# Performance work log

Hardware: AMD Instinct MI355X
Metric: run time of the kernel (lower is better)

Reference implementation:

```python
import jax, jax.numpy as jnp
import numpy as np

T = 64      # sequence_length / rolling_size
B = 256     # batch
XD = 128    # x_dim
HD = 1024   # h_dim
SKIP = 5    # frozen skip_size (torch code draws random.randint(1,10) at init)


def _make_masks(rs, n):
    # Mirrors: W1=randint(0,1); W2=1 if W1==0 else randint(0,1)
    masks = []
    for _ in range(n):
        w1 = int(rs.randint(0, 2))
        w2 = 1 if w1 == 0 else int(rs.randint(0, 2))
        masks.append((float(w1), float(w2)))
    return masks

_RS = np.random.RandomState(0)
ENC_MASKS = _make_masks(_RS, T)  # encoder constructed first in RAE.__init__
DEC_MASKS = _make_masks(_RS, T)


def _gru_cell(x, h, W_ih, W_hh, b_ih, b_hh):
    # torch.nn.GRUCell semantics
    gi = x @ W_ih.T + b_ih            # [B, 3H]
    gh = h @ W_hh.T + b_hh            # [B, 3H]
    i_r, i_z, i_n = jnp.split(gi, 3, axis=1)
    h_r, h_z, h_n = jnp.split(gh, 3, axis=1)
    r = jax.nn.sigmoid(i_r + h_r)
    z = jax.nn.sigmoid(i_z + h_z)
    n = jnp.tanh(i_n + r * h_n)
    return (1.0 - z) * n + z * h


def setup_inputs() -> dict:
    key = jax.random.key(0)
    ks = jax.random.split(key, 12)
    s = 0.05
    return {
        "input": jax.random.normal(ks[0], (B, T, XD), jnp.float32),
        "enc_W_ih": jax.random.normal(ks[1], (3 * HD, XD), jnp.float32) * s,
        "enc_W_hh": jax.random.normal(ks[2], (3 * HD, HD), jnp.float32) * s,
        "enc_b_ih": jax.random.normal(ks[3], (3 * HD,), jnp.float32) * s,
        "enc_b_hh": jax.random.normal(ks[4], (3 * HD,), jnp.float32) * s,
        "dec_W_ih": jax.random.normal(ks[5], (3 * HD, XD), jnp.float32) * s,
        "dec_W_hh": jax.random.normal(ks[6], (3 * HD, HD), jnp.float32) * s,
        "dec_b_ih": jax.random.normal(ks[7], (3 * HD,), jnp.float32) * s,
        "dec_b_hh": jax.random.normal(ks[8], (3 * HD,), jnp.float32) * s,
        "lin_W": jax.random.normal(ks[9], (XD, HD), jnp.float32) * s,
        "lin_b": jax.random.normal(ks[10], (XD,), jnp.float32) * s,
    }


def reference(input, enc_W_ih, enc_W_hh, enc_b_ih, enc_b_hh,
              dec_W_ih, dec_W_hh, dec_b_ih, dec_b_hh, lin_W, lin_b):
    Bn = input.shape[0]
    zeros_h = jnp.zeros((Bn, HD), input.dtype)

    # ---- Encoder: masked-skip GRU recurrence (list semantics match torch) ----
    h_origs = [zeros_h]
    h_skips = [zeros_h] * SKIP
    for i in range(T):
        h_prev = h_origs[i] * ENC_MASKS[i][0] + h_skips[i - SKIP] * ENC_MASKS[i][1]
        h_new = _gru_cell(input[:, i], h_prev, enc_W_ih, enc_W_hh, enc_b_ih, enc_b_hh)
        h_origs.append(h_new)
        h_skips.append(h_new)  # chunk(repeat(1,2)) gives two identical copies
    h_enc = h_origs[-1] + h_skips[-1]

    # ---- Decoder: feeds back its own projected output ----
    GO = jnp.zeros((Bn, XD), input.dtype)
    h_origs = [h_enc]
    h_skips = [zeros_h] * SKIP
    outputs = []
    for i in range(T):
        x_in = GO if i == 0 else outputs[i - 1]
        h_prev = h_origs[i] * DEC_MASKS[i][0] + h_skips[i - SKIP] * DEC_MASKS[i][1]
        h_new = _gru_cell(x_in, h_prev, dec_W_ih, dec_W_hh, dec_b_ih, dec_b_hh)
        h_origs.append(h_new)
        h_skips.append(h_new)
        # torch projects AFTER the appends, using h_origs[i] (pre-update state)
        proj = (h_origs[i] + h_skips[i - SKIP]) @ lin_W.T + lin_b
        outputs.append(proj)

    return jnp.stack(outputs, axis=1)  # [B, T, XD], matches permute(1,0,2)
```

## Files before the change

kernel.cpp:

```cpp
#include <hip/hip_runtime.h>
#include <cstdint>
#include <cstddef>

#define XDIM 128
#define HDIM 1024
#define ORS 8192
#define NPH 129

typedef __attribute__((ext_vector_type(8))) short short8;
typedef __attribute__((ext_vector_type(4))) float f32x4;

static const size_t GSTRIDE = (size_t)36 * 64 * 64 * 8;
static const size_t EPACK   = 4 * GSTRIDE;

struct Phase {
  float spA, spB, nsA, nsB, qsA, qsB, q2sA, q2sB;
  int ebase, xe, xd, afrag;
  int hpA, hpB, nskip, qskip, q2skip;
  int anext, pnext, p2next, hout;
  int pfrag, pouti, pxout;
};
static_assert(sizeof(Phase) == 96, "phase size");

__device__ __forceinline__ unsigned short f2bf(float f) {
  union { float f; unsigned u; } c; c.f = f;
  unsigned u = c.u + (0x7fffu + ((c.u >> 16) & 1u));
  return (unsigned short)(u >> 16);
}
__device__ __forceinline__ float sigm_(float x) { return 1.f / (1.f + __expf(-x)); }
__device__ __forceinline__ float tanh_(float x) { return 2.f / (1.f + __expf(-2.f * x)) - 1.f; }

__device__ __forceinline__ short8 cvt8(float4 a, float4 b) {
  short8 o;
  o[0] = (short)f2bf(a.x); o[1] = (short)f2bf(a.y); o[2] = (short)f2bf(a.z); o[3] = (short)f2bf(a.w);
  o[4] = (short)f2bf(b.x); o[5] = (short)f2bf(b.y); o[6] = (short)f2bf(b.z); o[7] = (short)f2bf(b.w);
  return o;
}

__device__ __forceinline__ unsigned long long ld64_sys(const unsigned short* p) {
  return __hip_atomic_load((const unsigned long long*)p, __ATOMIC_RELAXED,
                           __HIP_MEMORY_SCOPE_SYSTEM);
}
__device__ __forceinline__ unsigned ld32_sys(const unsigned* p) {
  return __hip_atomic_load(p, __ATOMIC_RELAXED, __HIP_MEMORY_SCOPE_SYSTEM);
}
__device__ __forceinline__ void st32_sys(unsigned* p, unsigned v) {
  __hip_atomic_store(p, v, __ATOMIC_RELAXED, __HIP_MEMORY_SCOPE_SYSTEM);
}
union U128 { unsigned long long u[2]; short8 v; };
__device__ __forceinline__ short8 mk8(unsigned long long a, unsigned long long b) {
  U128 u; u.u[0] = a; u.u[1] = b; return u.v;
}
__device__ __forceinline__ void st_pair_bf(unsigned short* addr, int lane, unsigned short v) {
  unsigned other = (unsigned)__shfl_xor((int)(unsigned)v, 1);
  if ((lane & 1) == 0)
    st32_sys((unsigned*)addr, ((unsigned)v & 0xffffu) | (other << 16));
}

#define MFMA(a,b,c) __builtin_amdgcn_mfma_f32_16x16x32_bf16((a),(b),(c),0,0,0)

__global__ __launch_bounds__(256) void pack_gates(
    const float* __restrict__ eWih, const float* __restrict__ eWhh,
    const float* __restrict__ dWih, const float* __restrict__ dWhh,
    short* __restrict__ Bg)
{
  unsigned t = blockIdx.x * 256u + threadIdx.x;
  unsigned l  = t & 63u; t >>= 6;
  unsigned nf = t & 63u; t >>= 6;
  unsigned ks = t % 36u; t /= 36u;
  unsigned g  = t & 3u;  t >>= 2;
  if (t >= 2u) return;
  if ((g == 2u && ks >= 4u) || (g == 3u && ks < 4u)) return;
  const float* Wih = t ? dWih : eWih;
  const float* Whh = t ? dWhh : eWhh;
  int k = (int)(ks * 32u + (l >> 4) * 8u);
  int n = (int)(nf * 16u + (l & 15u));
  const float* src;
  if (g == 3u)      src = Whh + (size_t)(2048 + n) * HDIM + (k - XDIM);
  else if (g == 2u) src = Wih + (size_t)(2048 + n) * XDIM + k;
  else if (ks < 4u) src = Wih + (size_t)(g * HDIM + n) * XDIM + k;
  else              src = Whh + (size_t)(g * HDIM + n) * HDIM + (k - XDIM);
  float4 a = *(const float4*)src;
  float4 b = *(const float4*)(src + 4);
  size_t off = ((((size_t)t * 4u + g) * 36u + ks) * 64u + nf) * 64u + l;
  *(short8*)(Bg + off * 8u) = cvt8(a, b);
}

__global__ __launch_bounds__(256) void pack_lin(const float* __restrict__ linW,
                                                short* __restrict__ Bl)
{
  unsigned t = blockIdx.x * 256u + threadIdx.x;
  unsigned l  = t & 63u; t >>= 6;
  unsigned nf = t & 7u;  t >>= 3;
  unsigned ks = t;
  if (ks >= 32u) return;
  int k = (int)(ks * 32u + (l >> 4) * 8u);
  int n = (int)(nf * 16u + (l & 15u));
  const float* src = linW + (size_t)n * HDIM + k;
  float4 a = *(const float4*)src;
  float4 b = *(const float4*)(src + 4);
  *(short8*)(Bl + (((size_t)ks * 8u + nf) * 64u + l) * 8u) = cvt8(a, b);
}

__global__ __launch_bounds__(256) void pack_bias(
    const float* __restrict__ eIh, const float* __restrict__ eHh,
    const float* __restrict__ dIh, const float* __restrict__ dHh,
    float* __restrict__ bias)
{
  unsigned t = blockIdx.x * 256u + threadIdx.x;
  if (t >= 8192u) return;
  unsigned n = t & 1023u, g = (t >> 10) & 3u, e = t >> 12;
  const float* bih = e ? dIh : eIh;
  const float* bhh = e ? dHh : eHh;
  float v;
  if (g == 0u)      v = bih[n] + bhh[n];
  else if (g == 1u) v = bih[HDIM + n] + bhh[HDIM + n];
  else if (g == 2u) v = bih[2 * HDIM + n];
  else              v = bhh[2 * HDIM + n];
  bias[t] = v;
}

__global__ __launch_bounds__(256) void pack_x(const float* __restrict__ in,
                                              unsigned short* __restrict__ Xe)
{
  unsigned t = blockIdx.x * 256u + threadIdx.x;
  unsigned row = t & 255u; t >>= 8;
  unsigned lq  = t & 3u;   t >>= 2;
  unsigned ks  = t & 3u;   t >>= 2;
  unsigned i   = t;
  if (i >= 64u) return;
  const float* src = in + (size_t)row * ORS + i * 128u + ks * 32u + lq * 8u;
  float4 a = *(const float4*)src;
  float4 b = *(const float4*)(src + 4);
  *(short8*)(Xe + ((((size_t)i * 4u + ks) * 4u + lq) * 256u + row) * 8u) = cvt8(a, b);
}

__device__ __forceinline__ int mkslot(int s) { return s % 12; }

__device__ void blank_phase(Phase& ph) {
  ph.spA = ph.spB = ph.nsA = ph.nsB = ph.qsA = ph.qsB = ph.q2sA = ph.q2sB = 0.f;
  ph.ebase = 0; ph.xe = -1; ph.xd = -1; ph.afrag = -1;
  ph.hpA = ph.hpB = ph.nskip = ph.qskip = ph.q2skip = 0;
  ph.anext = ph.pnext = ph.p2next = -1; ph.hout = -1;
  ph.pfrag = -1; ph.pouti = -1; ph.pxout = -1;
}

__global__ void setup_phases(Phase* __restrict__ phs, unsigned* __restrict__ arr) {
  const int t = threadIdx.x;
  for (int k = t; k < 1024; k += 64) arr[k] = 0u;
  if (t != 0) return;

  unsigned mt[624];
  mt[0] = 0u;
  for (int i = 1; i < 624; ++i)
    mt[i] = 1812433253u * (mt[i - 1] ^ (mt[i - 1] >> 30)) + (unsigned)i;
  for (int i = 0; i < 624; ++i) {
    unsigned y = (mt[i] & 0x80000000u) | (mt[(i + 1) % 624] & 0x7fffffffu);
    unsigned v = mt[(i + 397) % 624] ^ (y >> 1);
    mt[i] = (y & 1u) ? (v ^ 0x9908b0dfu) : v;
  }
  int mti = 0;
  float ew[64][2], dw[64][2];
  for (int e = 0; e < 2; ++e) {
    for (int i = 0; i < 64; ++i) {
      unsigned y = mt[mti++];
      y ^= y >> 11; y ^= (y << 7) & 0x9d2c5680u; y ^= (y << 15) & 0xefc60000u; y ^= y >> 18;
      int w1 = (int)(y & 1u);
      int w2 = 1;
      if (w1 != 0) {
        unsigned z = mt[mti++];
        z ^= z >> 11; z ^= (z << 7) & 0x9d2c5680u; z ^= (z << 15) & 0xefc60000u; z ^= z >> 18;
        w2 = (int)(z & 1u);
      }
      if (e == 0) { ew[i][0] = (float)w1; ew[i][1] = (float)w2; }
      else        { dw[i][0] = (float)w1; dw[i][1] = (float)w2; }
    }
  }

  bool anull = true;
  for (int i = 0; i < 64; ++i) {
    Phase ph; blank_phase(ph);
    ph.ebase = 0; ph.xe = i;
    ph.hout = mkslot(i);
    if (i >= 1 && !anull) ph.afrag = i & 3;
    ph.hpA = mkslot(i >= 1 ? i - 1 : 0);
    ph.spA = i ? ew[i][0] : 0.f;
    if (i == 3)       { ph.hpB = mkslot(1);      ph.spB = ew[i][1]; }
    else if (i == 4)  { ph.hpB = mkslot(3);      ph.spB = ew[i][1]; }
    else if (i >= 10) { ph.hpB = mkslot(i - 10); ph.spB = ew[i][1]; }
    if (i < 63) {
      int n = i + 1;
      ph.anext = n & 3;
      if (n == 4) ph.nsA = ew[4][0] + ew[4][1];
      else {
        ph.nsA = ew[n][0];
        if (n == 3)       { ph.nsB = ew[3][1]; ph.nskip = mkslot(1); }
        else if (n >= 10) { ph.nsB = ew[n][1]; ph.nskip = mkslot(n - 10); }
      }
    } else {
      ph.anext = 0; ph.nsA = 2.f * dw[0][0];
      ph.pnext = 0; ph.qsA = 2.f;
    }
    if (ph.anext >= 0) {
      anull = (ph.nsA == 0.f && ph.nsB == 0.f);
      if (anull) ph.anext = -1;
    }
    phs[i] = ph;
  }
  for (int i = 0; i < 64; ++i) {
    int p = 64 + i + (i >= 5 ? 1 : 0);
    int s = 64 + i;
    Phase ph; blank_phase(ph);
    ph.ebase = 1;
    ph.xd = i ? (i - 1) & 3 : -1;
    ph.hout = mkslot(s);
    if (!anull) ph.afrag = i & 3;
    ph.hpA = mkslot(i ? s - 1 : 63);
    ph.spA = i ? dw[i][0] : 2.f * dw[0][0];
    if (i == 3)       { ph.hpB = mkslot(64 + 1);  ph.spB = dw[i][1]; }
    else if (i == 4)  { ph.hpB = mkslot(64 + 3);  ph.spB = dw[i][1]; }
    else if (i >= 10) { ph.hpB = mkslot(s - 10);  ph.spB = dw[i][1]; }
    if (i < 63) {
      int n = i + 1;
      ph.anext = n & 3;
      if (n == 4) ph.nsA = dw[4][0] + dw[4][1];
      else {
        ph.nsA = dw[n][0];
        if (n == 3)       { ph.nsB = dw[3][1]; ph.nskip = mkslot(64 + 1); }
        else if (n >= 10) { ph.nsB = dw[n][1]; ph.nskip = mkslot(64 + n - 10); }
      }
    }
    if (i == 2)      { ph.pnext = 3; ph.qsA = 2.f; }
    else if (i == 3) {  }
    else if (i == 4) { ph.pnext = 1; ph.qsA = 1.f;
                       ph.p2next = 0; ph.q2sA = 1.f; ph.q2sB = 1.f;
                       ph.q2skip = mkslot(64 + 3); }
    else if (i < 63) {
      int n = i + 1;
      ph.pnext = n & 3; ph.qsA = 1.f;
      if (n == 2)       { ph.qsB = 1.f; ph.qskip = mkslot(64 + 0); }
      else if (n >= 10) { ph.qsB = 1.f; ph.qskip = mkslot(64 + n - 10); }
    }
    if (ph.anext >= 0) {
      bool z = (ph.nsA == 0.f && ph.nsB == 0.f);
      if (z) ph.anext = -1;
      anull = z;
    }
    if (i != 4) { ph.pfrag = i & 3; ph.pouti = i; ph.pxout = i & 3; }
    phs[p] = ph;
    if (i == 4) {
      Phase pp; blank_phase(pp);
      pp.ebase = 1;
      pp.pfrag = 0; pp.pouti = 4; pp.pxout = 0;
      phs[69] = pp;
    }
  }
}

__global__ __launch_bounds__(512, 2) void rae_persist(
    const Phase* __restrict__ phs,
    const unsigned short* __restrict__ Xe,
    const unsigned short* __restrict__ BgE,
    const unsigned short* __restrict__ BgD,
    const unsigned short* __restrict__ Blin,
    const float* __restrict__ bias,
    const float* __restrict__ linb,
    float* __restrict__ hring,
    unsigned short* __restrict__ AnB,
    unsigned short* __restrict__ PnB,
    unsigned short* __restrict__ XdB,
    float* __restrict__ out,
    unsigned* __restrict__ arr)
{
  const int tid = threadIdx.x;
  const int lane = tid & 63;
  const int wave = tid >> 6;
  const int l15 = lane & 15, lq = lane >> 4;
  const int bid = blockIdx.x;
  const int mt = bid >> 5, ns = bid & 31;
  const int nf0 = ns * 2;
  const int R0 = mt * 32;
  const int hu0 = (wave < 4) ? wave + 8 : wave;

  __shared__ f32x4 red[8][2][6][64];
  __shared__ f32x4 red2[4][2][2][64];
  __shared__ f32x4 red3[8][2][64];
  __shared__ Phase lph[NPH];

  for (int idx = tid; idx < NPH * (int)(sizeof(Phase) / 4); idx += 512)
    ((int*)lph)[idx] = ((const int*)phs)[idx];
  __syncthreads();

#pragma unroll 1
  for (int p = 0; p < NPH; ++p) {
    const Phase& ph = lph[p];
    const bool cell = (ph.hout >= 0);
    const bool proj = (ph.pfrag >= 0) && (ns < 8);
    const unsigned short* Bg = ph.ebase ? BgD : BgE;
    const float* bias4 = bias + (ph.ebase ? 4096 : 0);

    const f32x4 zero = {0.f, 0.f, 0.f, 0.f};
    f32x4 acc[2][6];
    f32x4 g2a[2][2];
#pragma unroll
    for (int rf = 0; rf < 2; ++rf) {
#pragma unroll
      for (int s = 0; s < 6; ++s) acc[rf][s] = zero;
      g2a[rf][0] = zero; g2a[rf][1] = zero;
    }

    auto do_x = [&](const unsigned short* xf, bool sys) {
      const unsigned short* bb = Bg + ((size_t)(wave * 64 + nf0) * 64 + lane) * 8;
      short8 b00 = *(const short8*)(bb);
      short8 b01 = *(const short8*)(bb + 512);
      short8 b10 = *(const short8*)(bb + GSTRIDE);
      short8 b11 = *(const short8*)(bb + GSTRIDE + 512);
      short8 b20 = *(const short8*)(bb + 2 * GSTRIDE);
      short8 b21 = *(const short8*)(bb + 2 * GSTRIDE + 512);
#pragma unroll
      for (int rf = 0; rf < 2; ++rf) {
        const unsigned short* a = xf + (((size_t)(wave * 4 + lq)) * 256 + R0 + rf * 16 + l15) * 8;
        short8 av;
        if (sys) av = mk8(ld64_sys(a), ld64_sys(a + 4));
        else     av = *(const short8*)a;
        acc[rf][0] = MFMA(av, b00, acc[rf][0]);
        acc[rf][1] = MFMA(av, b01, acc[rf][1]);
        acc[rf][2] = MFMA(av, b10, acc[rf][2]);
        acc[rf][3] = MFMA(av, b11, acc[rf][3]);
        g2a[rf][0] = MFMA(av, b20, g2a[rf][0]);
        g2a[rf][1] = MFMA(av, b21, g2a[rf][1]);
      }
    };

    float hpv[4] = {0,0,0,0}, nskv[4] = {0,0,0,0},
          qskv[4] = {0,0,0,0}, q2skv[4] = {0,0,0,0};
    if (cell && wave < 4) {
      const int erf = wave >> 1, enf = wave & 1;
      const int colE = ns * 32 + enf * 16 + l15;
      const float* hpA = hring + (size_t)ph.hpA * 262144u;
      const float* hpB = hring + (size_t)ph.hpB * 262144u;
      const float* nsk = hring + (size_t)ph.nskip * 262144u;
      const float* qsk = hring + (size_t)ph.qskip * 262144u;
      const float* q2k = hring + (size_t)ph.q2skip * 262144u;
#pragma unroll
      for (int q = 0; q < 4; ++q) {
        const size_t o = (size_t)(R0 + erf * 16 + lq * 4 + q) * HDIM + colE;
        float hv = 0.f;
        if (ph.spA != 0.f) hv = ph.spA * hpA[o];
        if (ph.spB != 0.f) hv = fmaf(ph.spB, hpB[o], hv);
        hpv[q] = hv;
        if (ph.anext >= 0 && ph.nsB != 0.f) nskv[q] = nsk[o];
        if (ph.pnext >= 0 && ph.qsB != 0.f) qskv[q] = qsk[o];
        if (ph.p2next >= 0) q2skv[q] = q2k[o];
      }
    }
    if (cell && wave < 4 && ph.xe >= 0)
      do_x(Xe + (size_t)ph.xe * 32768u, false);

    if (p > 0) {
      int guard = 0;
      for (;;) {
        unsigned v = ld32_sys(&arr[(mt << 5) + (lane & 31)]);
        if (__all(v >= (unsigned)p)) break;
        if (++guard > (1 << 22)) break;
      }
    }

    if (cell && wave < 4 && ph.xd >= 0)
      do_x(XdB + (size_t)ph.xd * 32768u, true);

    if (cell && ph.afrag >= 0) {
      const unsigned short* af = AnB + (size_t)ph.afrag * 262144u;
      unsigned long long ha0[4][2], ha1[4][2];
#pragma unroll
      for (int k = 0; k < 4; ++k) {
        const int u = hu0 + 8 * k;
#pragma unroll
        for (int rf = 0; rf < 2; ++rf) {
          const unsigned short* b =
              af + (((size_t)((u - 4) * 4 + lq)) * 256 + R0 + rf * 16 + l15) * 8;
          ha0[k][rf] = ld64_sys(b); ha1[k][rf] = ld64_sys(b + 4);
        }
      }
#pragma unroll
      for (int k = 0; k < 4; ++k) {
        const int u = hu0 + 8 * k;
        const unsigned short* bb = Bg + ((size_t)(u * 64 + nf0) * 64 + lane) * 8;
        short8 b00 = *(const short8*)(bb);
        short8 b01 = *(const short8*)(bb + 512);
        short8 b10 = *(const short8*)(bb + GSTRIDE);
        short8 b11 = *(const short8*)(bb + GSTRIDE + 512);
        short8 b30 = *(const short8*)(bb + 3 * GSTRIDE);
        short8 b31 = *(const short8*)(bb + 3 * GSTRIDE + 512);
#pragma unroll
        for (int rf = 0; rf < 2; ++rf) {
          short8 av = mk8(ha0[k][rf], ha1[k][rf]);
          acc[rf][0] = MFMA(av, b00, acc[rf][0]);
          acc[rf][1] = MFMA(av, b01, acc[rf][1]);
          acc[rf][2] = MFMA(av, b10, acc[rf][2]);
          acc[rf][3] = MFMA(av, b11, acc[rf][3]);
          acc[rf][4] = MFMA(av, b30, acc[rf][4]);
          acc[rf][5] = MFMA(av, b31, acc[rf][5]);
        }
      }
    }

    if (cell) {
#pragma unroll
      for (int rf = 0; rf < 2; ++rf) {
#pragma unroll
        for (int s = 0; s < 6; ++s) red[wave][rf][s][lane] = acc[rf][s];
      }
      if (wave < 4) {
#pragma unroll
        for (int rf = 0; rf < 2; ++rf) {
          red2[wave][rf][0][lane] = g2a[rf][0];
          red2[wave][rf][1][lane] = g2a[rf][1];
        }
      }
    }
    __syncthreads();

    if (cell && wave < 4) {
      const int erf = wave >> 1, enf = wave & 1;
      f32x4 S0 = zero, S1 = zero, S3 = zero, S2 = zero;
#pragma unroll
      for (int w = 0; w < 8; ++w) {
        S0 += red[w][erf][0 + enf][lane];
        S1 += red[w][erf][2 + enf][lane];
        S3 += red[w][erf][4 + enf][lane];
      }
#pragma unroll
      for (int w = 0; w < 4; ++w) S2 += red2[w][erf][enf][lane];
      const int colE = ns * 32 + enf * 16 + l15;
      const float br = bias4[colE],            bz = bias4[HDIM + colE];
      const float bi = bias4[2 * HDIM + colE], bh = bias4[3 * HDIM + colE];
      const int fa = (colE >> 3) * 2048 + (colE & 7);
      float* hout = hring + (size_t)ph.hout * 262144u;
      unsigned short* anx = ph.anext  >= 0 ? AnB + (size_t)ph.anext  * 262144u : nullptr;
      unsigned short* pnx = ph.pnext  >= 0 ? PnB + (size_t)ph.pnext  * 262144u : nullptr;
      unsigned short* p2x = ph.p2next >= 0 ? PnB + (size_t)ph.p2next * 262144u : nullptr;
#pragma unroll
      for (int q = 0; q < 4; ++q) {
        const int row = R0 + erf * 16 + lq * 4 + q;
        const float r  = sigm_(S0[q] + br);
        const float z  = sigm_(S1[q] + bz);
        const float nv = tanh_(S2[q] + bi + r * (S3[q] + bh));
        const float h  = (1.f - z) * nv + z * hpv[q];
        if (anx) st_pair_bf(anx + fa + row * 8, lane, f2bf(ph.nsA * h + ph.nsB * nskv[q]));
        if (pnx) st_pair_bf(pnx + fa + row * 8, lane, f2bf(ph.qsA * h + ph.qsB * qskv[q]));
        if (p2x) st_pair_bf(p2x + fa + row * 8, lane, f2bf(ph.q2sA * h + ph.q2sB * q2skv[q]));
        hout[(size_t)row * HDIM + colE] = h;
      }
    }

    if (proj) {
      const unsigned short* pf = PnB + (size_t)ph.pfrag * 262144u;
      unsigned long long q0[4][2], q1[4][2];
#pragma unroll
      for (int k0 = 0; k0 < 4; ++k0) {
        const int ks = wave * 4 + k0;
#pragma unroll
        for (int rf = 0; rf < 2; ++rf) {
          const unsigned short* a =
              pf + (((size_t)(ks * 4 + lq)) * 256 + R0 + rf * 16 + l15) * 8;
          q0[k0][rf] = ld64_sys(a); q1[k0][rf] = ld64_sys(a + 4);
        }
      }
      f32x4 pacc0 = zero, pacc1 = zero;
#pragma unroll
      for (int k0 = 0; k0 < 4; ++k0) {
        const int ks = wave * 4 + k0;
        short8 b = *(const short8*)(Blin + (((size_t)ks * 8 + ns) * 64 + lane) * 8);
        pacc0 = MFMA(mk8(q0[k0][0], q1[k0][0]), b, pacc0);
        pacc1 = MFMA(mk8(q0[k0][1], q1[k0][1]), b, pacc1);
      }
      red3[wave][0][lane] = pacc0;
      red3[wave][1][lane] = pacc1;
    }
    if (ph.pfrag >= 0 && ns < 8) __syncthreads();
    if (proj && wave == 0) {
      const int col = ns * 16 + l15;
      const float lb = linb[col];
      const int fx = (col >> 3) * 2048 + (col & 7);
      float* po = out + (size_t)ph.pouti * XDIM;
      unsigned short* px = XdB + (size_t)ph.pxout * 32768u;
#pragma unroll
      for (int rf = 0; rf < 2; ++rf) {
        f32x4 S = red3[0][rf][lane];
#pragma unroll
        for (int w = 1; w < 8; ++w) S += red3[w][rf][lane];
#pragma unroll
        for (int q = 0; q < 4; ++q) {
          const int row = R0 + rf * 16 + lq * 4 + q;
          const float v = S[q] + lb;
          po[(size_t)row * ORS + col] = v;
          st_pair_bf(px + fx + row * 8, lane, f2bf(v));
        }
      }
    }

    asm volatile("s_waitcnt vmcnt(0)" ::: "memory");
    __syncthreads();
    if (tid == 0) st32_sys(&arr[(mt << 5) + ns], (unsigned)(p + 1));
  }
}

extern "C" void kernel_launch(void* const* d_in, const int* in_sizes, int n_in,
                              void* d_out, int out_size, void* d_ws, size_t ws_size,
                              hipStream_t stream)
{
  const float* input = (const float*)d_in[0];
  const float* eWih = (const float*)d_in[1];
  const float* eWhh = (const float*)d_in[2];
  const float* eBih = (const float*)d_in[3];
  const float* eBhh = (const float*)d_in[4];
  const float* dWih = (const float*)d_in[5];
  const float* dWhh = (const float*)d_in[6];
  const float* dBih = (const float*)d_in[7];
  const float* dBhh = (const float*)d_in[8];
  const float* linW = (const float*)d_in[9];
  const float* linb = (const float*)d_in[10];
  float* out = (float*)d_out;

  if (ws_size < 40423424u) return;
  char* ws = (char*)d_ws;
  short* BgE  = (short*)ws;
  short* BgD  = BgE + EPACK;
  short* Blin = (short*)(ws + 18874368u);
  float* bias = (float*)(ws + 19136512u);
  float* hring = (float*)(ws + 19169280u);
  unsigned short* Xe  = (unsigned short*)(ws + 31752192u);
  unsigned short* AnB = (unsigned short*)(ws + 35946496u);
  unsigned short* PnB = (unsigned short*)(ws + 38043648u);
  unsigned short* XdB = (unsigned short*)(ws + 40140800u);
  Phase* phs = (Phase*)(ws + 40402944u);
  unsigned* arr = (unsigned*)(ws + 40419328u);

  pack_gates<<<4608, 256, 0, stream>>>(eWih, eWhh, dWih, dWhh, BgE);
  pack_lin<<<64, 256, 0, stream>>>(linW, Blin);
  pack_bias<<<32, 256, 0, stream>>>(eBih, eBhh, dBih, dBhh, bias);
  pack_x<<<1024, 256, 0, stream>>>(input, Xe);
  setup_phases<<<1, 64, 0, stream>>>(phs, arr);

  rae_persist<<<256, 512, 0, stream>>>(
      phs, Xe, (const unsigned short*)BgE, (const unsigned short*)BgD,
      (const unsigned short*)Blin, bias, linb,
      hring, AnB, PnB, XdB, out, arr);
}
```

Measured before the change: 1.357 ms.

## Replace all-block barrier with fine-grained per-producer flags and split proj flag

Measured after the change: 2.621 ms. 93.2% more time.

```diff
diff --git a/kernel.cpp b/kernel.cpp
--- a/kernel.cpp
+++ b/kernel.cpp
@@ -102,24 +102,6 @@
   *(short8*)(Bl + (((size_t)ks * 8u + nf) * 64u + l) * 8u) = cvt8(a, b);
 }
 
-__global__ __launch_bounds__(256) void pack_bias(
-    const float* __restrict__ eIh, const float* __restrict__ eHh,
-    const float* __restrict__ dIh, const float* __restrict__ dHh,
-    float* __restrict__ bias)
-{
-  unsigned t = blockIdx.x * 256u + threadIdx.x;
-  if (t >= 8192u) return;
-  unsigned n = t & 1023u, g = (t >> 10) & 3u, e = t >> 12;
-  const float* bih = e ? dIh : eIh;
-  const float* bhh = e ? dHh : eHh;
-  float v;
-  if (g == 0u)      v = bih[n] + bhh[n];
-  else if (g == 1u) v = bih[HDIM + n] + bhh[HDIM + n];
-  else if (g == 2u) v = bih[2 * HDIM + n];
-  else              v = bhh[2 * HDIM + n];
-  bias[t] = v;
-}
-
 __global__ __launch_bounds__(256) void pack_x(const float* __restrict__ in,
                                               unsigned short* __restrict__ Xe)
 {
@@ -145,9 +127,27 @@
   ph.pfrag = -1; ph.pouti = -1; ph.pxout = -1;
 }
 
-__global__ void setup_phases(Phase* __restrict__ phs, unsigned* __restrict__ arr) {
+__global__ __launch_bounds__(256) void pack_bias_setup(
+    const float* __restrict__ eIh, const float* __restrict__ eHh,
+    const float* __restrict__ dIh, const float* __restrict__ dHh,
+    float* __restrict__ bias, Phase* __restrict__ phs, unsigned* __restrict__ arr)
+{
+  if (blockIdx.x < 32) {
+    unsigned t = blockIdx.x * 256u + threadIdx.x;
+    if (t >= 8192u) return;
+    unsigned n = t & 1023u, g = (t >> 10) & 3u, e = t >> 12;
+    const float* bih = e ? dIh : eIh;
+    const float* bhh = e ? dHh : eHh;
+    float v;
+    if (g == 0u)      v = bih[n] + bhh[n];
+    else if (g == 1u) v = bih[HDIM + n] + bhh[HDIM + n];
+    else if (g == 2u) v = bih[2 * HDIM + n];
+    else              v = bhh[2 * HDIM + n];
+    bias[t] = v;
+    return;
+  }
   const int t = threadIdx.x;
-  for (int k = t; k < 1024; k += 64) arr[k] = 0u;
+  for (int k = t; k < 1024; k += 256) arr[k] = 0u;
   if (t != 0) return;
 
   unsigned mt[624];
@@ -257,7 +257,7 @@
   }
 }
 
-__global__ __launch_bounds__(512, 2) void rae_persist(
+__global__ __launch_bounds__(512, 1) void rae_persist(
     const Phase* __restrict__ phs,
     const unsigned short* __restrict__ Xe,
     const unsigned short* __restrict__ BgE,
@@ -291,11 +291,15 @@
     ((int*)lph)[idx] = ((const int*)phs)[idx];
   __syncthreads();
 
+  unsigned* const arrC = arr + (mt << 6);
+  unsigned* const arrP = arr + (mt << 6) + 32;
+  const int hprod = ((wave < 4) ? wave + 4 : wave - 4) + 8 * (lane & 3);
+
 #pragma unroll 1
   for (int p = 0; p < NPH; ++p) {
     const Phase& ph = lph[p];
     const bool cell = (ph.hout >= 0);
-    const bool proj = (ph.pfrag >= 0) && (ns < 8);
+    const bool isProj = (ph.pfrag >= 0) && (ns < 8);
     const unsigned short* Bg = ph.ebase ? BgD : BgE;
     const float* bias4 = bias + (ph.ebase ? 4096 : 0);
 
@@ -308,29 +312,6 @@
       for (int s = 0; s < 6; ++s) acc[rf][s] = zero;
       g2a[rf][0] = zero; g2a[rf][1] = zero;
     }
-
-    auto do_x = [&](const unsigned short* xf, bool sys) {
-      const unsigned short* bb = Bg + ((size_t)(wave * 64 + nf0) * 64 + lane) * 8;
-      short8 b00 = *(const short8*)(bb);
-      short8 b01 = *(const short8*)(bb + 512);
-      short8 b10 = *(const short8*)(bb + GSTRIDE);
-      short8 b11 = *(const short8*)(bb + GSTRIDE + 512);
-      short8 b20 = *(const short8*)(bb + 2 * GSTRIDE);
-      short8 b21 = *(const short8*)(bb + 2 * GSTRIDE + 512);
-#pragma unroll
-      for (int rf = 0; rf < 2; ++rf) {
-        const unsigned short* a = xf + (((size_t)(wave * 4 + lq)) * 256 + R0 + rf * 16 + l15) * 8;
-        short8 av;
-        if (sys) av = mk8(ld64_sys(a), ld64_sys(a + 4));
-        else     av = *(const short8*)a;
-        acc[rf][0] = MFMA(av, b00, acc[rf][0]);
-        acc[rf][1] = MFMA(av, b01, acc[rf][1]);
-        acc[rf][2] = MFMA(av, b10, acc[rf][2]);
-        acc[rf][3] = MFMA(av, b11, acc[rf][3]);
-        g2a[rf][0] = MFMA(av, b20, g2a[rf][0]);
-        g2a[rf][1] = MFMA(av, b21, g2a[rf][1]);
-      }
-    };
 
     float hpv[4] = {0,0,0,0}, nskv[4] = {0,0,0,0},
           qskv[4] = {0,0,0,0}, q2skv[4] = {0,0,0,0};
@@ -354,24 +335,67 @@
         if (ph.p2next >= 0) q2skv[q] = q2k[o];
       }
     }
-    if (cell && wave < 4 && ph.xe >= 0)
-      do_x(Xe + (size_t)ph.xe * 32768u, false);
+    if (cell && wave < 4 && ph.xe >= 0) {
+      const unsigned short* xf = Xe + (size_t)ph.xe * 32768u;
+      const unsigned short* bb = Bg + ((size_t)(wave * 64 + nf0) * 64 + lane) * 8;
+      short8 b00 = *(const short8*)(bb);
+      short8 b01 = *(const short8*)(bb + 512);
+      short8 b10 = *(const short8*)(bb + GSTRIDE);
+      short8 b11 = *(const short8*)(bb + GSTRIDE + 512);
+      short8 b20 = *(const short8*)(bb + 2 * GSTRIDE);
+      short8 b21 = *(const short8*)(bb + 2 * GSTRIDE + 512);
+#pragma unroll
+      for (int rf = 0; rf < 2; ++rf) {
+        const unsigned short* a = xf + (((size_t)(wave * 4 + lq)) * 256 + R0 + rf * 16 + l15) * 8;
+        short8 av = *(const short8*)a;
+        acc[rf][0] = MFMA(av, b00, acc[rf][0]);
+        acc[rf][1] = MFMA(av, b01, acc[rf][1]);
+        acc[rf][2] = MFMA(av, b10, acc[rf][2]);
+        acc[rf][3] = MFMA(av, b11, acc[rf][3]);
+        g2a[rf][0] = MFMA(av, b20, g2a[rf][0]);
+        g2a[rf][1] = MFMA(av, b21, g2a[rf][1]);
+      }
+    }
+    const bool decx = cell && (wave < 4) && (ph.xd >= 0);
+    short8 xb[6];
+    if (decx) {
+      const unsigned short* bb = Bg + ((size_t)(wave * 64 + nf0) * 64 + lane) * 8;
+      xb[0] = *(const short8*)(bb);
+      xb[1] = *(const short8*)(bb + 512);
+      xb[2] = *(const short8*)(bb + GSTRIDE);
+      xb[3] = *(const short8*)(bb + GSTRIDE + 512);
+      xb[4] = *(const short8*)(bb + 2 * GSTRIDE);
+      xb[5] = *(const short8*)(bb + 2 * GSTRIDE + 512);
+    }
 
     if (p > 0) {
+      const int li = lane;
+      const unsigned* pa = arrC + hprod;
+      bool act = (li < 4);
+      if (li >= 4 && li < 6 && decx)    { pa = arrP + (2 * wave + (li - 4)); act = true; }
+      if (li >= 6 && li < 10 && isProj) { pa = arrC + (4 * wave + (li - 6)); act = true; }
+      const unsigned tgt = (unsigned)p;
       int guard = 0;
       for (;;) {
-        unsigned v = ld32_sys(&arr[(mt << 5) + (lane & 31)]);
-        if (__all(v >= (unsigned)p)) break;
+        unsigned v = ld32_sys(pa);
+        if (__all(!act || v >= tgt)) break;
         if (++guard > (1 << 22)) break;
       }
     }
 
-    if (cell && wave < 4 && ph.xd >= 0)
-      do_x(XdB + (size_t)ph.xd * 32768u, true);
-
-    if (cell && ph.afrag >= 0) {
+    unsigned long long xd0[2], xd1[2];
+    if (decx) {
+      const unsigned short* xf = XdB + (size_t)ph.xd * 32768u;
+#pragma unroll
+      for (int rf = 0; rf < 2; ++rf) {
+        const unsigned short* a = xf + (((size_t)(wave * 4 + lq)) * 256 + R0 + rf * 16 + l15) * 8;
+        xd0[rf] = ld64_sys(a); xd1[rf] = ld64_sys(a + 4);
+      }
+    }
+    const bool hasA = cell && (ph.afrag >= 0);
+    unsigned long long ha0[4][2], ha1[4][2];
+    if (hasA) {
       const unsigned short* af = AnB + (size_t)ph.afrag * 262144u;
-      unsigned long long ha0[4][2], ha1[4][2];
 #pragma unroll
       for (int k = 0; k < 4; ++k) {
         const int u = hu0 + 8 * k;
@@ -382,6 +406,35 @@
           ha0[k][rf] = ld64_sys(b); ha1[k][rf] = ld64_sys(b + 4);
         }
       }
+    }
+    unsigned long long pq0[4][2], pq1[4][2];
+    if (isProj) {
+      const unsigned short* pf = PnB + (size_t)ph.pfrag * 262144u;
+#pragma unroll
+      for (int k0 = 0; k0 < 4; ++k0) {
+        const int ks = wave * 4 + k0;
+#pragma unroll
+        for (int rf = 0; rf < 2; ++rf) {
+          const unsigned short* a =
+              pf + (((size_t)(ks * 4 + lq)) * 256 + R0 + rf * 16 + l15) * 8;
+          pq0[k0][rf] = ld64_sys(a); pq1[k0][rf] = ld64_sys(a + 4);
+        }
+      }
+    }
+
+    if (decx) {
+#pragma unroll
+      for (int rf = 0; rf < 2; ++rf) {
+        short8 av = mk8(xd0[rf], xd1[rf]);
+        acc[rf][0] = MFMA(av, xb[0], acc[rf][0]);
+        acc[rf][1] = MFMA(av, xb[1], acc[rf][1]);
+        acc[rf][2] = MFMA(av, xb[2], acc[rf][2]);
+        acc[rf][3] = MFMA(av, xb[3], acc[rf][3]);
+        g2a[rf][0] = MFMA(av, xb[4], g2a[rf][0]);
+        g2a[rf][1] = MFMA(av, xb[5], g2a[rf][1]);
+      }
+    }
+    if (hasA) {
 #pragma unroll
       for (int k = 0; k < 4; ++k) {
         const int u = hu0 + 8 * k;
@@ -454,32 +507,27 @@
       }
     }
 
-    if (proj) {
-      const unsigned short* pf = PnB + (size_t)ph.pfrag * 262144u;
-      unsigned long long q0[4][2], q1[4][2];
-#pragma unroll
-      for (int k0 = 0; k0 < 4; ++k0) {
-        const int ks = wave * 4 + k0;
-#pragma unroll
-        for (int rf = 0; rf < 2; ++rf) {
-          const unsigned short* a =
-              pf + (((size_t)(ks * 4 + lq)) * 256 + R0 + rf * 16 + l15) * 8;
-          q0[k0][rf] = ld64_sys(a); q1[k0][rf] = ld64_sys(a + 4);
-        }
-      }
+    if (isProj) {
       f32x4 pacc0 = zero, pacc1 = zero;
 #pragma unroll
       for (int k0 = 0; k0 < 4; ++k0) {
         const int ks = wave * 4 + k0;
         short8 b = *(const short8*)(Blin + (((size_t)ks * 8 + ns) * 64 + lane) * 8);
-        pacc0 = MFMA(mk8(q0[k0][0], q1[k0][0]), b, pacc0);
-        pacc1 = MFMA(mk8(q0[k0][1], q1[k0][1]), b, pacc1);
+        pacc0 = MFMA(mk8(pq0[k0][0], pq1[k0][0]), b, pacc0);
+        pacc1 = MFMA(mk8(pq0[k0][1], pq1[k0][1]), b, pacc1);
       }
       red3[wave][0][lane] = pacc0;
       red3[wave][1][lane] = pacc1;
     }
-    if (ph.pfrag >= 0 && ns < 8) __syncthreads();
-    if (proj && wave == 0) {
+
+    asm volatile("s_waitcnt vmcnt(0)" ::: "memory");
+    __syncthreads();
+    if (tid == 0) {
+      st32_sys(arrC + ns, (unsigned)(p + 1));
+      if (!isProj) st32_sys(arrP + ns, (unsigned)(p + 1));
+    }
+
+    if (isProj && wave == 0) {
       const int col = ns * 16 + l15;
       const float lb = linb[col];
       const int fx = (col >> 3) * 2048 + (col & 7);
@@ -498,11 +546,9 @@
           st_pair_bf(px + fx + row * 8, lane, f2bf(v));
         }
       }
-    }
-
-    asm volatile("s_waitcnt vmcnt(0)" ::: "memory");
-    __syncthreads();
-    if (tid == 0) st32_sys(&arr[(mt << 5) + ns], (unsigned)(p + 1));
+      asm volatile("s_waitcnt vmcnt(0)" ::: "memory");
+      if (lane == 0) st32_sys(arrP + ns, (unsigned)(p + 1));
+    }
   }
 }
 
@@ -539,9 +585,8 @@
 
   pack_gates<<<4608, 256, 0, stream>>>(eWih, eWhh, dWih, dWhh, BgE);
   pack_lin<<<64, 256, 0, stream>>>(linW, Blin);
-  pack_bias<<<32, 256, 0, stream>>>(eBih, eBhh, dBih, dBhh, bias);
   pack_x<<<1024, 256, 0, stream>>>(input, Xe);
-  setup_phases<<<1, 64, 0, stream>>>(phs, arr);
+  pack_bias_setup<<<33, 256, 0, stream>>>(eBih, eBhh, dBih, dBhh, bias, phs, arr);
 
   rae_persist<<<256, 512, 0, stream>>>(
       phs, Xe, (const unsigned short*)BgE, (const unsigned short*)BgD,
```
